# Optimization experiments

Hardware: AMD Instinct MI355X
Metric: run time of the kernel (lower is better)

Reference implementation:

```python
import jax, jax.numpy as jnp
import numpy as np
from jax.scipy.special import logsumexp

ALPHA = 1.0
TOP_K = 128
SK_EPS = 0.001   # sinkhorn entropic epsilon
SK_ITERS = 20    # max_iter (thresh early-exit dropped for jit; 20 fixed iters)
CLIP_MIN = 0.0001


def _cdist(x, y):
    # batched Euclidean distance, safe-sqrt so grad at 0 is 0 (matches torch.cdist subgradient)
    d2 = (jnp.sum(x * x, -1)[..., :, None] + jnp.sum(y * y, -1)[..., None, :]
          - 2.0 * jnp.einsum('bnd,bmd->bnm', x, y))
    d2 = jnp.maximum(d2, 0.0)
    safe = jnp.where(d2 > 0, d2, 1.0)
    return jnp.where(d2 > 0, jnp.sqrt(safe), 0.0)


def _sinkhorn(cost, p, q):
    # log-domain entropic OT with marginals p [B,N], q [B,M]
    logp, logq = jnp.log(p), jnp.log(q)

    def M(u, v):
        return (-cost + u[..., :, None] + v[..., None, :]) / SK_EPS

    def body(carry, _):
        u, v = carry
        u = SK_EPS * (logp - logsumexp(M(u, v), axis=-1)) + u
        v = SK_EPS * (logq - logsumexp(M(u, v), axis=-2)) + v
        return (u, v), None

    u0 = jnp.zeros_like(p)
    v0 = jnp.zeros_like(q)
    (u, v), _ = jax.lax.scan(body, (u0, v0), None, length=SK_ITERS)
    return jnp.exp(M(u, v))  # transport plan gamma [B,N,M]


def setup_inputs() -> dict:
    key = jax.random.key(0)
    ks = jax.random.split(key, 6)
    B, N, M, D = 8, 2048, 2048, 256
    return {
        'src': jax.random.normal(ks[0], (B, N, 3), dtype=jnp.float32),
        'tgt': jax.random.normal(ks[1], (B, M, 3), dtype=jnp.float32),
        'src_feats': jax.random.normal(ks[2], (B, N, D), dtype=jnp.float32),
        'tgt_feats': jax.random.uniform(ks[3], (B, M, D), dtype=jnp.float32),
        'src_o': jax.random.uniform(ks[4], (B, N), dtype=jnp.float32),
        'tgt_o': jax.random.uniform(ks[5], (B, M), dtype=jnp.float32),
    }


def reference(src, tgt, src_feats, tgt_feats, src_o, tgt_o):
    src_pi = src_o / jnp.maximum(jnp.sum(src_o, -1, keepdims=True), CLIP_MIN)
    tgt_pi = tgt_o / jnp.maximum(jnp.sum(tgt_o, -1, keepdims=True), CLIP_MIN)
    cost = _cdist(src_feats, tgt_feats)                       # [B,N,M]
    gamma = _sinkhorn(cost, src_pi, tgt_pi)                   # [B,N,M]
    src_corr = (jnp.einsum('bnm,bmd->bnd', gamma, tgt)
                / jnp.maximum(jnp.sum(gamma, -1, keepdims=True), CLIP_MIN))
    prob = jnp.max(gamma, axis=-1)                            # [B,N]
    _, idx = jax.lax.top_k(prob, TOP_K)                       # [B,K]
    src_k = jnp.take_along_axis(src, idx[:, :, None], axis=1)       # [B,K,3]
    tgt_k = jnp.take_along_axis(src_corr, idx[:, :, None], axis=1)  # [B,K,3]
    alpha2 = ALPHA * ALPHA
    src_edge = _cdist(src_k, src_k)
    tgt_edge = _cdist(tgt_k, tgt_k)
    z = jnp.abs(src_edge - tgt_edge)
    loss = jnp.sum(1.0 - jnp.exp(-0.5 * z * z / alpha2), axis=-1)
    return jnp.mean(loss)
```

## Files before the change

kernel.cpp:

```cpp
#include <hip/hip_runtime.h>
#include <math.h>

#define Bb 8
#define Nn 2048
#define Mm 2048
#define Dd 256
#define TOPK 128
#define SK_ITERS 20
#define NCH 32
#define CHROWS (Nn/NCH)
#define NEG_INIT (-1e30f)
#define SCALE_L2 (-1442.6950408889634f)

__global__ void wl_init_kernel(const float* __restrict__ src_o, const float* __restrict__ tgt_o,
                               float* __restrict__ logp2, float* __restrict__ logq2,
                               float* __restrict__ Ve) {
    __shared__ float lds[8];
    int b = blockIdx.x, t = threadIdx.x;
    int l = t & 63, w = t >> 6;
    float s = 0.f, q = 0.f;
    for (int i = t; i < Nn; i += 256) s += src_o[b * Nn + i];
    for (int i = t; i < Mm; i += 256) q += tgt_o[b * Mm + i];
    for (int o = 32; o; o >>= 1) { s += __shfl_xor(s, o); q += __shfl_xor(q, o); }
    if (l == 0) { lds[w] = s; lds[4 + w] = q; }
    __syncthreads();
    float ssum = fmaxf(lds[0] + lds[1] + lds[2] + lds[3], 1e-4f);
    float qsum = fmaxf(lds[4] + lds[5] + lds[6] + lds[7], 1e-4f);
    float rs = 1.f / ssum, rq = 1.f / qsum;
    for (int i = t; i < Nn; i += 256) logp2[b * Nn + i] = log2f(src_o[b * Nn + i] * rs);
    for (int i = t; i < Mm; i += 256) { logq2[b * Mm + i] = log2f(tgt_o[b * Mm + i] * rq); Ve[b * Mm + i] = 0.f; }
}

__global__ void wl_norms_kernel(const float* __restrict__ feats, float* __restrict__ out) {
    int w = threadIdx.x >> 6, l = threadIdx.x & 63;
    int row = blockIdx.x * 4 + w;
    float4 f = ((const float4*)(feats + (size_t)row * Dd))[l];
    float s = f.x * f.x + f.y * f.y + f.z * f.z + f.w * f.w;
    for (int o = 32; o; o >>= 1) s += __shfl_xor(s, o);
    if (l == 0) out[row] = s;
}

#define BT 128
#define KT 32
#define LDT 132
__global__ __launch_bounds__(256)
void wl_cost_kernel(const float* __restrict__ A, const float* __restrict__ Bf,
                    const float* __restrict__ nx, const float* __restrict__ ny,
                    float* __restrict__ Sc) {
    __shared__ float As[KT][LDT];
    __shared__ float Bs[KT][LDT];
    int b = blockIdx.z;
    int n0 = blockIdx.y * BT, m0 = blockIdx.x * BT;
    const float* Ab = A + (size_t)b * Nn * Dd;
    const float* Bbp = Bf + (size_t)b * Mm * Dd;
    int t = threadIdx.x;
    int w = t >> 6, l = t & 63;
    int tx = (w & 1) * 8 + (l & 7);
    int ty = (w >> 1) * 8 + (l >> 3);
    float acc[8][8] = {};
    for (int k0 = 0; k0 < Dd; k0 += KT) {
        __syncthreads();
#pragma unroll
        for (int i = 0; i < 4; i++) {
            int c = t + 256 * i;
            int row = c >> 3, kc = (c & 7) << 2;
            float4 v = *(const float4*)(Ab + (size_t)(n0 + row) * Dd + k0 + kc);
            As[kc + 0][row] = v.x; As[kc + 1][row] = v.y; As[kc + 2][row] = v.z; As[kc + 3][row] = v.w;
            float4 u = *(const float4*)(Bbp + (size_t)(m0 + row) * Dd + k0 + kc);
            Bs[kc + 0][row] = u.x; Bs[kc + 1][row] = u.y; Bs[kc + 2][row] = u.z; Bs[kc + 3][row] = u.w;
        }
        __syncthreads();
#pragma unroll 4
        for (int k = 0; k < KT; k++) {
            float4 a0 = *(const float4*)&As[k][ty * 8];
            float4 a1 = *(const float4*)&As[k][ty * 8 + 4];
            float4 b0 = *(const float4*)&Bs[k][tx * 8];
            float4 b1 = *(const float4*)&Bs[k][tx * 8 + 4];
            float a[8] = { a0.x, a0.y, a0.z, a0.w, a1.x, a1.y, a1.z, a1.w };
            float bv[8] = { b0.x, b0.y, b0.z, b0.w, b1.x, b1.y, b1.z, b1.w };
#pragma unroll
            for (int i = 0; i < 8; i++)
#pragma unroll
                for (int j = 0; j < 8; j++)
                    acc[i][j] = fmaf(a[i], bv[j], acc[i][j]);
        }
    }
    float nyv[8];
#pragma unroll
    for (int j = 0; j < 8; j++) nyv[j] = ny[b * Mm + m0 + tx * 8 + j];
#pragma unroll
    for (int i = 0; i < 8; i++) {
        int n = n0 + ty * 8 + i;
        float nxv = nx[b * Nn + n];
        float o[8];
#pragma unroll
        for (int j = 0; j < 8; j++) {
            float d2 = nxv + nyv[j] - 2.f * acc[i][j];
            d2 = fmaxf(d2, 0.f);
            float c = d2 > 0.f ? sqrtf(d2) : 0.f;
            o[j] = SCALE_L2 * c;
        }
        float* orow = Sc + ((size_t)b * Nn + n) * Mm + m0 + tx * 8;
        *(float4*)orow = make_float4(o[0], o[1], o[2], o[3]);
        *(float4*)(orow + 4) = make_float4(o[4], o[5], o[6], o[7]);
    }
}

__global__ __launch_bounds__(256)
void wl_u_kernel(const float* __restrict__ Sc, const float* __restrict__ Ve,
                 const float* __restrict__ logp2, float* __restrict__ Ue) {
    int w = threadIdx.x >> 6, l = threadIdx.x & 63;
    int row = blockIdx.x * 4 + w;
    int b = row >> 11;
    const float4* s4 = (const float4*)(Sc + (size_t)row * Mm);
    const float4* v4 = (const float4*)(Ve + (size_t)b * Mm);
    float mx0 = NEG_INIT, mx1 = NEG_INIT, mx2 = NEG_INIT, mx3 = NEG_INIT;
    float sm0 = 0.f, sm1 = 0.f, sm2 = 0.f, sm3 = 0.f;
#pragma unroll
    for (int i = 0; i < 8; i++) {
        int c = l + 64 * i;
        float4 sv = s4[c]; float4 vv = v4[c];
        float t0 = sv.x + vv.x, t1 = sv.y + vv.y, t2 = sv.z + vv.z, t3 = sv.w + vv.w;
        float n0 = fmaxf(mx0, t0); sm0 = sm0 * exp2f(mx0 - n0) + exp2f(t0 - n0); mx0 = n0;
        float n1 = fmaxf(mx1, t1); sm1 = sm1 * exp2f(mx1 - n1) + exp2f(t1 - n1); mx1 = n1;
        float n2 = fmaxf(mx2, t2); sm2 = sm2 * exp2f(mx2 - n2) + exp2f(t2 - n2); mx2 = n2;
        float n3 = fmaxf(mx3, t3); sm3 = sm3 * exp2f(mx3 - n3) + exp2f(t3 - n3); mx3 = n3;
    }
    float mx = fmaxf(fmaxf(mx0, mx1), fmaxf(mx2, mx3));
    float sm = sm0 * exp2f(mx0 - mx) + sm1 * exp2f(mx1 - mx) + sm2 * exp2f(mx2 - mx) + sm3 * exp2f(mx3 - mx);
    for (int o = 32; o; o >>= 1) {
        float om = __shfl_xor(mx, o), os = __shfl_xor(sm, o);
        float nm = fmaxf(mx, om);
        sm = sm * exp2f(mx - nm) + os * exp2f(om - nm);
        mx = nm;
    }
    if (l == 0) Ue[row] = logp2[row] - (mx + log2f(sm));
}

__global__ __launch_bounds__(256)
void wl_v_partial_kernel(const float* __restrict__ Sc, const float* __restrict__ Ue,
                         float* __restrict__ pmx, float* __restrict__ psm) {
    int b = blockIdx.z, ch = blockIdx.y;
    int m0 = blockIdx.x * 1024 + threadIdx.x * 4;
    const float* base = Sc + (size_t)b * Nn * Mm;
    const float* ue = Ue + b * Nn;
    float mx0 = NEG_INIT, mx1 = NEG_INIT, mx2 = NEG_INIT, mx3 = NEG_INIT;
    float sm0 = 0.f, sm1 = 0.f, sm2 = 0.f, sm3 = 0.f;
    int nst = ch * CHROWS;
#pragma unroll 4
    for (int n = nst; n < nst + CHROWS; n++) {
        float u = ue[n];
        float4 sv = *(const float4*)(base + (size_t)n * Mm + m0);
        float t0 = sv.x + u, t1 = sv.y + u, t2 = sv.z + u, t3 = sv.w + u;
        float n0 = fmaxf(mx0, t0); sm0 = sm0 * exp2f(mx0 - n0) + exp2f(t0 - n0); mx0 = n0;
        float n1 = fmaxf(mx1, t1); sm1 = sm1 * exp2f(mx1 - n1) + exp2f(t1 - n1); mx1 = n1;
        float n2 = fmaxf(mx2, t2); sm2 = sm2 * exp2f(mx2 - n2) + exp2f(t2 - n2); mx2 = n2;
        float n3 = fmaxf(mx3, t3); sm3 = sm3 * exp2f(mx3 - n3) + exp2f(t3 - n3); mx3 = n3;
    }
    size_t pi = ((size_t)(b * NCH + ch)) * Mm + m0;
    *(float4*)(pmx + pi) = make_float4(mx0, mx1, mx2, mx3);
    *(float4*)(psm + pi) = make_float4(sm0, sm1, sm2, sm3);
}

__global__ void wl_v_combine_kernel(const float* __restrict__ pmx, const float* __restrict__ psm,
                                    const float* __restrict__ logq2, float* __restrict__ Ve) {
    int idx = blockIdx.x * 256 + threadIdx.x;
    int b = idx >> 11, m = idx & (Mm - 1);
    float mx = NEG_INIT, sm = 0.f;
#pragma unroll
    for (int ch = 0; ch < NCH; ch++) {
        float om = pmx[((size_t)(b * NCH + ch)) * Mm + m];
        float os = psm[((size_t)(b * NCH + ch)) * Mm + m];
        float nm = fmaxf(mx, om);
        sm = sm * exp2f(mx - nm) + os * exp2f(om - nm);
        mx = nm;
    }
    Ve[idx] = logq2[idx] - (mx + log2f(sm));
}

__global__ __launch_bounds__(256)
void wl_finalize_kernel(const float* __restrict__ Sc, const float* __restrict__ Ue,
                        const float* __restrict__ Ve, const float* __restrict__ tgt,
                        float* __restrict__ prob, float* __restrict__ corr) {
    int w = threadIdx.x >> 6, l = threadIdx.x & 63;
    int row = blockIdx.x * 4 + w;
    int b = row >> 11;
    const float4* s4 = (const float4*)(Sc + (size_t)row * Mm);
    const float4* v4 = (const float4*)(Ve + (size_t)b * Mm);
    const float4* tg4 = (const float4*)(tgt + (size_t)b * Mm * 3);
    float mx = NEG_INIT, sm = 0.f, w0 = 0.f, w1 = 0.f, w2 = 0.f;
#pragma unroll
    for (int i = 0; i < 8; i++) {
        int c = l + 64 * i;
        float4 sv = s4[c]; float4 vv = v4[c];
        float4 g0 = tg4[3 * c + 0], g1 = tg4[3 * c + 1], g2 = tg4[3 * c + 2];
        float tt[4] = { sv.x + vv.x, sv.y + vv.y, sv.z + vv.z, sv.w + vv.w };
        float gx[4] = { g0.x, g0.w, g1.z, g2.y };
        float gy[4] = { g0.y, g1.x, g1.w, g2.z };
        float gz[4] = { g0.z, g1.y, g2.x, g2.w };
#pragma unroll
        for (int j = 0; j < 4; j++) {
            float nm = fmaxf(mx, tt[j]);
            float ce = exp2f(mx - nm), e = exp2f(tt[j] - nm);
            sm = sm * ce + e;
            w0 = w0 * ce + e * gx[j];
            w1 = w1 * ce + e * gy[j];
            w2 = w2 * ce + e * gz[j];
            mx = nm;
        }
    }
    for (int o = 32; o; o >>= 1) {
        float om = __shfl_xor(mx, o), os = __shfl_xor(sm, o);
        float o0 = __shfl_xor(w0, o), o1 = __shfl_xor(w1, o), o2 = __shfl_xor(w2, o);
        float nm = fmaxf(mx, om);
        float c1 = exp2f(mx - nm), c2 = exp2f(om - nm);
        sm = sm * c1 + os * c2;
        w0 = w0 * c1 + o0 * c2;
        w1 = w1 * c1 + o1 * c2;
        w2 = w2 * c1 + o2 * c2;
        mx = nm;
    }
    if (l == 0) {
        float scale = exp2f(Ue[row] + mx);
        float rowsum = scale * sm;
        float den = fmaxf(rowsum, 1e-4f);
        prob[row] = scale;
        corr[(size_t)row * 3 + 0] = scale * w0 / den;
        corr[(size_t)row * 3 + 1] = scale * w1 / den;
        corr[(size_t)row * 3 + 2] = scale * w2 / den;
    }
}

__global__ __launch_bounds__(256)
void wl_topk_kernel(const float* __restrict__ prob, int* __restrict__ topk) {
    __shared__ float key[2048];
    __shared__ int val[2048];
    int b = blockIdx.x, t = threadIdx.x;
    for (int i = t; i < 2048; i += 256) { key[i] = prob[b * 2048 + i]; val[i] = i; }
    __syncthreads();
    for (int size = 2; size <= 2048; size <<= 1) {
        for (int stride = size >> 1; stride > 0; stride >>= 1) {
            for (int q = t; q < 1024; q += 256) {
                int i = 2 * q - (q & (stride - 1));
                int j = i + stride;
                bool up = ((i & size) == 0);
                float ki = key[i], kj = key[j];
                int vi = val[i], vj = val[j];
                bool jBetter = (kj > ki) || (kj == ki && vj < vi);
                if (up ? jBetter : !jBetter) {
                    key[i] = kj; key[j] = ki;
                    val[i] = vj; val[j] = vi;
                }
            }
            __syncthreads();
        }
    }
    if (t < TOPK) topk[b * TOPK + t] = val[t];
}

__global__ __launch_bounds__(256)
void wl_edge_kernel(const float* __restrict__ src, const float* __restrict__ corr,
                    const int* __restrict__ topk, float* __restrict__ bloss) {
    __shared__ float sx[TOPK][3];
    __shared__ float tx[TOPK][3];
    __shared__ float lds[4];
    int b = blockIdx.x, t = threadIdx.x;
    if (t < TOPK) {
        int id = topk[b * TOPK + t];
        sx[t][0] = src[((size_t)b * 2048 + id) * 3 + 0];
        sx[t][1] = src[((size_t)b * 2048 + id) * 3 + 1];
        sx[t][2] = src[((size_t)b * 2048 + id) * 3 + 2];
        tx[t][0] = corr[((size_t)b * 2048 + id) * 3 + 0];
        tx[t][1] = corr[((size_t)b * 2048 + id) * 3 + 1];
        tx[t][2] = corr[((size_t)b * 2048 + id) * 3 + 2];
    }
    __syncthreads();
    float acc = 0.f;
    for (int p = t; p < TOPK * TOPK; p += 256) {
        int i = p >> 7, j = p & 127;
        float dx = sx[i][0] - sx[j][0], dy = sx[i][1] - sx[j][1], dz = sx[i][2] - sx[j][2];
        float d2s = dx * dx + dy * dy + dz * dz;
        float ds = d2s > 0.f ? sqrtf(d2s) : 0.f;
        float ex = tx[i][0] - tx[j][0], ey = tx[i][1] - tx[j][1], ez = tx[i][2] - tx[j][2];
        float d2t = ex * ex + ey * ey + ez * ez;
        float dt = d2t > 0.f ? sqrtf(d2t) : 0.f;
        float z = fabsf(ds - dt);
        acc += 1.f - expf(-0.5f * z * z);
    }
    int l = t & 63, w = t >> 6;
    for (int o = 32; o; o >>= 1) acc += __shfl_xor(acc, o);
    if (l == 0) lds[w] = acc;
    __syncthreads();
    if (t == 0) bloss[b] = lds[0] + lds[1] + lds[2] + lds[3];
}

__global__ void wl_final_kernel(const float* __restrict__ bloss, float* __restrict__ out) {
    if (threadIdx.x == 0) {
        float s = 0.f;
        for (int i = 0; i < Bb; i++) s += bloss[i];
        out[0] = s / 1024.f;
    }
}

extern "C" void kernel_launch(void* const* d_in, const int* in_sizes, int n_in,
                              void* d_out, int out_size, void* d_ws, size_t ws_size,
                              hipStream_t stream) {
    (void)in_sizes; (void)n_in; (void)out_size;
    const float* src       = (const float*)d_in[0];
    const float* tgt       = (const float*)d_in[1];
    const float* src_feats = (const float*)d_in[2];
    const float* tgt_feats = (const float*)d_in[3];
    const float* src_o     = (const float*)d_in[4];
    const float* tgt_o     = (const float*)d_in[5];
    float* out = (float*)d_out;

    float* ws = (float*)d_ws;
    size_t off = 0;
    float* Sc    = ws + off; off += (size_t)Bb * Nn * Mm;
    float* Ue    = ws + off; off += Bb * Nn;
    float* Ve    = ws + off; off += Bb * Mm;
    float* logp2 = ws + off; off += Bb * Nn;
    float* logq2 = ws + off; off += Bb * Mm;
    float* nx    = ws + off; off += Bb * Nn;
    float* ny    = ws + off; off += Bb * Mm;
    float* prob  = ws + off; off += Bb * Nn;
    float* corr  = ws + off; off += (size_t)Bb * Nn * 3;
    float* pmx   = ws + off; off += (size_t)Bb * NCH * Mm;
    float* psm   = ws + off; off += (size_t)Bb * NCH * Mm;
    int*   topk  = (int*)(ws + off); off += Bb * TOPK;
    float* bloss = ws + off; off += Bb;
    if (ws_size < off * sizeof(float)) return;

    wl_init_kernel<<<Bb, 256, 0, stream>>>(src_o, tgt_o, logp2, logq2, Ve);
    wl_norms_kernel<<<(Bb * Nn) / 4, 256, 0, stream>>>(src_feats, nx);
    wl_norms_kernel<<<(Bb * Mm) / 4, 256, 0, stream>>>(tgt_feats, ny);
    wl_cost_kernel<<<dim3(Mm / BT, Nn / BT, Bb), 256, 0, stream>>>(src_feats, tgt_feats, nx, ny, Sc);

    for (int it = 0; it < SK_ITERS; it++) {
        wl_u_kernel<<<(Bb * Nn) / 4, 256, 0, stream>>>(Sc, Ve, logp2, Ue);
        wl_v_partial_kernel<<<dim3(Mm / 1024, NCH, Bb), 256, 0, stream>>>(Sc, Ue, pmx, psm);
        wl_v_combine_kernel<<<(Bb * Mm) / 256, 256, 0, stream>>>(pmx, psm, logq2, Ve);
    }

    wl_finalize_kernel<<<(Bb * Nn) / 4, 256, 0, stream>>>(Sc, Ue, Ve, tgt, prob, corr);
    wl_topk_kernel<<<Bb, 256, 0, stream>>>(prob, topk);
    wl_edge_kernel<<<Bb, 256, 0, stream>>>(src, corr, topk, bloss);
    wl_final_kernel<<<1, 64, 0, stream>>>(bloss, out);
}
```

Measured before the change: 1.459 ms.

## Fuse Sinkhorn u-update and v-partial reduction into one pass over cost matrix

Merges the row logsumexp (u update) and the column partial logsumexp into a single kernel, so each iteration reads the 128MB cost matrix once instead of twice. Each wave takes a strip of rows, computes the row LSE, and folds the u-shifted values into per-column running max/sum registers. The partials are merged across waves in LDS, and the chunk count goes to 64 when the workspace is large enough. The v-combine now adds the old V, since the partials are taken relative to it. This uses many registers (64 accumulators plus 32 temporaries per thread) and launches only 256 or 512 blocks, which may reduce occupancy.

Measured after the change: 1.867 ms. 28.0% more time.

```diff
diff --git a/kernel.cpp b/kernel.cpp
--- a/kernel.cpp
+++ b/kernel.cpp
@@ -7,10 +7,16 @@
 #define Dd 256
 #define TOPK 128
 #define SK_ITERS 20
-#define NCH 32
-#define CHROWS (Nn/NCH)
 #define NEG_INIT (-1e30f)
 #define SCALE_L2 (-1442.6950408889634f)
+
+__device__ __forceinline__ void lse_merge(float& m, float& s, float m2, float s2) {
+    float d = m2 - m;
+    float e = exp2f(-fabsf(d));
+    bool up = (d > 0.f);
+    s = up ? fmaf(s, e, s2) : fmaf(s2, e, s);
+    m = up ? m2 : m;
+}
 
 __global__ void wl_init_kernel(const float* __restrict__ src_o, const float* __restrict__ tgt_o,
                                float* __restrict__ logp2, float* __restrict__ logq2,
@@ -106,76 +112,85 @@
     }
 }
 
-__global__ __launch_bounds__(256)
-void wl_u_kernel(const float* __restrict__ Sc, const float* __restrict__ Ve,
-                 const float* __restrict__ logp2, float* __restrict__ Ue) {
-    int w = threadIdx.x >> 6, l = threadIdx.x & 63;
-    int row = blockIdx.x * 4 + w;
-    int b = row >> 11;
-    const float4* s4 = (const float4*)(Sc + (size_t)row * Mm);
-    const float4* v4 = (const float4*)(Ve + (size_t)b * Mm);
-    float mx0 = NEG_INIT, mx1 = NEG_INIT, mx2 = NEG_INIT, mx3 = NEG_INIT;
-    float sm0 = 0.f, sm1 = 0.f, sm2 = 0.f, sm3 = 0.f;
-#pragma unroll
-    for (int i = 0; i < 8; i++) {
-        int c = l + 64 * i;
-        float4 sv = s4[c]; float4 vv = v4[c];
-        float t0 = sv.x + vv.x, t1 = sv.y + vv.y, t2 = sv.z + vv.z, t3 = sv.w + vv.w;
-        float n0 = fmaxf(mx0, t0); sm0 = sm0 * exp2f(mx0 - n0) + exp2f(t0 - n0); mx0 = n0;
-        float n1 = fmaxf(mx1, t1); sm1 = sm1 * exp2f(mx1 - n1) + exp2f(t1 - n1); mx1 = n1;
-        float n2 = fmaxf(mx2, t2); sm2 = sm2 * exp2f(mx2 - n2) + exp2f(t2 - n2); mx2 = n2;
-        float n3 = fmaxf(mx3, t3); sm3 = sm3 * exp2f(mx3 - n3) + exp2f(t3 - n3); mx3 = n3;
-    }
-    float mx = fmaxf(fmaxf(mx0, mx1), fmaxf(mx2, mx3));
-    float sm = sm0 * exp2f(mx0 - mx) + sm1 * exp2f(mx1 - mx) + sm2 * exp2f(mx2 - mx) + sm3 * exp2f(mx3 - mx);
-    for (int o = 32; o; o >>= 1) {
-        float om = __shfl_xor(mx, o), os = __shfl_xor(sm, o);
-        float nm = fmaxf(mx, om);
-        sm = sm * exp2f(mx - nm) + os * exp2f(om - nm);
-        mx = nm;
-    }
-    if (l == 0) Ue[row] = logp2[row] - (mx + log2f(sm));
-}
-
-__global__ __launch_bounds__(256)
-void wl_v_partial_kernel(const float* __restrict__ Sc, const float* __restrict__ Ue,
-                         float* __restrict__ pmx, float* __restrict__ psm) {
-    int b = blockIdx.z, ch = blockIdx.y;
-    int m0 = blockIdx.x * 1024 + threadIdx.x * 4;
-    const float* base = Sc + (size_t)b * Nn * Mm;
-    const float* ue = Ue + b * Nn;
-    float mx0 = NEG_INIT, mx1 = NEG_INIT, mx2 = NEG_INIT, mx3 = NEG_INIT;
-    float sm0 = 0.f, sm1 = 0.f, sm2 = 0.f, sm3 = 0.f;
-    int nst = ch * CHROWS;
-#pragma unroll 4
-    for (int n = nst; n < nst + CHROWS; n++) {
-        float u = ue[n];
-        float4 sv = *(const float4*)(base + (size_t)n * Mm + m0);
-        float t0 = sv.x + u, t1 = sv.y + u, t2 = sv.z + u, t3 = sv.w + u;
-        float n0 = fmaxf(mx0, t0); sm0 = sm0 * exp2f(mx0 - n0) + exp2f(t0 - n0); mx0 = n0;
-        float n1 = fmaxf(mx1, t1); sm1 = sm1 * exp2f(mx1 - n1) + exp2f(t1 - n1); mx1 = n1;
-        float n2 = fmaxf(mx2, t2); sm2 = sm2 * exp2f(mx2 - n2) + exp2f(t2 - n2); mx2 = n2;
-        float n3 = fmaxf(mx3, t3); sm3 = sm3 * exp2f(mx3 - n3) + exp2f(t3 - n3); mx3 = n3;
-    }
-    size_t pi = ((size_t)(b * NCH + ch)) * Mm + m0;
-    *(float4*)(pmx + pi) = make_float4(mx0, mx1, mx2, mx3);
-    *(float4*)(psm + pi) = make_float4(sm0, sm1, sm2, sm3);
+__global__ __launch_bounds__(512, 4)
+void wl_fused_kernel(const float* __restrict__ Sc, const float* __restrict__ Ve,
+                     const float* __restrict__ logp2, float* __restrict__ Ue,
+                     float* __restrict__ pmx, float* __restrict__ psm, int nch) {
+    __shared__ float vlds[2048];
+    __shared__ float pm4[8][512];
+    __shared__ float ps4[8][512];
+    int b = blockIdx.y, ch = blockIdx.x;
+    int t = threadIdx.x, w = t >> 6, l = t & 63;
+
+    ((float4*)vlds)[t] = ((const float4*)(Ve + b * Mm))[t];
+    __syncthreads();
+
+    int chrows = Nn / nch;
+    int rpw = chrows >> 3;
+    int row0 = ch * chrows + w * rpw;
+
+    float cmx[32], csm[32];
+#pragma unroll
+    for (int j = 0; j < 32; j++) { cmx[j] = NEG_INIT; csm[j] = 0.f; }
+
+    for (int r = 0; r < rpw; r++) {
+        int row = row0 + r;
+        const float4* rp = (const float4*)(Sc + ((size_t)b * Nn + row) * Mm);
+        float tv[32];
+#pragma unroll
+        for (int j = 0; j < 8; j++) {
+            float4 sv = rp[l + 64 * j];
+            float4 vv = ((const float4*)vlds)[l + 64 * j];
+            tv[4 * j + 0] = sv.x + vv.x;
+            tv[4 * j + 1] = sv.y + vv.y;
+            tv[4 * j + 2] = sv.z + vv.z;
+            tv[4 * j + 3] = sv.w + vv.w;
+        }
+        float rm = tv[0];
+#pragma unroll
+        for (int j = 1; j < 32; j++) rm = fmaxf(rm, tv[j]);
+        for (int o = 32; o; o >>= 1) rm = fmaxf(rm, __shfl_xor(rm, o));
+        float rs = 0.f;
+#pragma unroll
+        for (int j = 0; j < 32; j++) rs += exp2f(tv[j] - rm);
+        for (int o = 32; o; o >>= 1) rs += __shfl_xor(rs, o);
+        float lp = logp2[b * Nn + row];
+        float lrs = log2f(rs);
+        if (l == 0) Ue[b * Nn + row] = lp - rm - lrs;
+        float C = lp - lrs - rm;
+#pragma unroll
+        for (int j = 0; j < 32; j++) lse_merge(cmx[j], csm[j], tv[j] + C, 1.f);
+    }
+
+    for (int q = 0; q < 4; q++) {
+        __syncthreads();
+#pragma unroll
+        for (int jj = 0; jj < 2; jj++) {
+            int j = 2 * q + jj;
+            *(float4*)&pm4[w][256 * jj + 4 * l] =
+                make_float4(cmx[4 * j + 0], cmx[4 * j + 1], cmx[4 * j + 2], cmx[4 * j + 3]);
+            *(float4*)&ps4[w][256 * jj + 4 * l] =
+                make_float4(csm[4 * j + 0], csm[4 * j + 1], csm[4 * j + 2], csm[4 * j + 3]);
+        }
+        __syncthreads();
+        float m = pm4[0][t], s = ps4[0][t];
+#pragma unroll
+        for (int ww = 1; ww < 8; ww++) lse_merge(m, s, pm4[ww][t], ps4[ww][t]);
+        size_t gi = ((size_t)(b * nch + ch)) * Mm + 512 * q + t;
+        pmx[gi] = m; psm[gi] = s;
+    }
 }
 
 __global__ void wl_v_combine_kernel(const float* __restrict__ pmx, const float* __restrict__ psm,
-                                    const float* __restrict__ logq2, float* __restrict__ Ve) {
+                                    const float* __restrict__ logq2, float* __restrict__ Ve, int nch) {
     int idx = blockIdx.x * 256 + threadIdx.x;
     int b = idx >> 11, m = idx & (Mm - 1);
     float mx = NEG_INIT, sm = 0.f;
-#pragma unroll
-    for (int ch = 0; ch < NCH; ch++) {
-        float om = pmx[((size_t)(b * NCH + ch)) * Mm + m];
-        float os = psm[((size_t)(b * NCH + ch)) * Mm + m];
-        float nm = fmaxf(mx, om);
-        sm = sm * exp2f(mx - nm) + os * exp2f(om - nm);
-        mx = nm;
-    }
-    Ve[idx] = logq2[idx] - (mx + log2f(sm));
+    for (int ch = 0; ch < nch; ch++) {
+        size_t gi = ((size_t)(b * nch + ch)) * Mm + m;
+        lse_merge(mx, sm, pmx[gi], psm[gi]);
+    }
+    Ve[idx] = logq2[idx] + Ve[idx] - mx - log2f(sm);
 }
 
 __global__ __launch_bounds__(256)
@@ -314,6 +329,10 @@
     const float* tgt_o     = (const float*)d_in[5];
     float* out = (float*)d_out;
 
+    size_t fixed = (size_t)Bb * Nn * Mm + 7 * (size_t)Bb * Nn + 3 * (size_t)Bb * Nn
+                 + (size_t)Bb * TOPK + Bb + 64;
+    int nch = (ws_size >= (fixed + 2 * (size_t)Bb * 64 * Mm) * sizeof(float)) ? 64 : 32;
+
     float* ws = (float*)d_ws;
     size_t off = 0;
     float* Sc    = ws + off; off += (size_t)Bb * Nn * Mm;
@@ -325,8 +344,8 @@
     float* ny    = ws + off; off += Bb * Mm;
     float* prob  = ws + off; off += Bb * Nn;
     float* corr  = ws + off; off += (size_t)Bb * Nn * 3;
-    float* pmx   = ws + off; off += (size_t)Bb * NCH * Mm;
-    float* psm   = ws + off; off += (size_t)Bb * NCH * Mm;
+    float* pmx   = ws + off; off += (size_t)Bb * nch * Mm;
+    float* psm   = ws + off; off += (size_t)Bb * nch * Mm;
     int*   topk  = (int*)(ws + off); off += Bb * TOPK;
     float* bloss = ws + off; off += Bb;
     if (ws_size < off * sizeof(float)) return;
@@ -337,9 +356,8 @@
     wl_cost_kernel<<<dim3(Mm / BT, Nn / BT, Bb), 256, 0, stream>>>(src_feats, tgt_feats, nx, ny, Sc);
 
     for (int it = 0; it < SK_ITERS; it++) {
-        wl_u_kernel<<<(Bb * Nn) / 4, 256, 0, stream>>>(Sc, Ve, logp2, Ue);
-        wl_v_partial_kernel<<<dim3(Mm / 1024, NCH, Bb), 256, 0, stream>>>(Sc, Ue, pmx, psm);
-        wl_v_combine_kernel<<<(Bb * Mm) / 256, 256, 0, stream>>>(pmx, psm, logq2, Ve);
+        wl_fused_kernel<<<dim3(nch, Bb), 512, 0, stream>>>(Sc, Ve, logp2, Ue, pmx, psm, nch);
+        wl_v_combine_kernel<<<(Bb * Mm) / 256, 256, 0, stream>>>(pmx, psm, logq2, Ve, nch);
     }
 
     wl_finalize_kernel<<<(Bb * Nn) / 4, 256, 0, stream>>>(Sc, Ue, Ve, tgt, prob, corr);
```

## Compute cost matrix with split-fp16 MFMA instead of scalar FP32 FMA

Applied to the files above, without the earlier changes.

The FP32 SIMT GEMM in the cost kernel is replaced by MFMA 16x16x32 f16 instructions. Each float is split into a high fp16 part and a scaled low fp16 residual, and three MFMA products are accumulated to approximate FP32 precision. Tiles become 64x128, and the output is stored as scalar writes in the MFMA layout. This targets the GEMM portion, which is a small share next to the 20 Sinkhorn passes over the 128MB cost matrix. Precision is slightly reduced, and the uncoalesced-ish scalar stores could add cost.

Result: faster. 1.363 ms (-6.5%).

```diff
diff --git a/kernel.cpp b/kernel.cpp
--- a/kernel.cpp
+++ b/kernel.cpp
@@ -11,6 +11,9 @@
 #define CHROWS (Nn/NCH)
 #define NEG_INIT (-1e30f)
 #define SCALE_L2 (-1442.6950408889634f)
+
+typedef _Float16 half8 __attribute__((ext_vector_type(8)));
+typedef float f32x4 __attribute__((ext_vector_type(4)));
 
 __global__ void wl_init_kernel(const float* __restrict__ src_o, const float* __restrict__ tgt_o,
                                float* __restrict__ logp2, float* __restrict__ logq2,
@@ -40,69 +43,92 @@
     if (l == 0) out[row] = s;
 }
 
-#define BT 128
-#define KT 32
-#define LDT 132
+#define CBM 64
+#define CBN 128
+#define CKT 32
+#define HPITCH 40
 __global__ __launch_bounds__(256)
 void wl_cost_kernel(const float* __restrict__ A, const float* __restrict__ Bf,
                     const float* __restrict__ nx, const float* __restrict__ ny,
                     float* __restrict__ Sc) {
-    __shared__ float As[KT][LDT];
-    __shared__ float Bs[KT][LDT];
+    __shared__ _Float16 Ah[CBM][HPITCH], Al[CBM][HPITCH];
+    __shared__ _Float16 Bh[CBN][HPITCH], Bl[CBN][HPITCH];
     int b = blockIdx.z;
-    int n0 = blockIdx.y * BT, m0 = blockIdx.x * BT;
+    int n0 = blockIdx.y * CBM, m0 = blockIdx.x * CBN;
     const float* Ab = A + (size_t)b * Nn * Dd;
     const float* Bbp = Bf + (size_t)b * Mm * Dd;
-    int t = threadIdx.x;
-    int w = t >> 6, l = t & 63;
-    int tx = (w & 1) * 8 + (l & 7);
-    int ty = (w >> 1) * 8 + (l >> 3);
-    float acc[8][8] = {};
-    for (int k0 = 0; k0 < Dd; k0 += KT) {
+    int t = threadIdx.x, w = t >> 6, l = t & 63;
+
+    f32x4 acc1[8], acc2[8];
+#pragma unroll
+    for (int c = 0; c < 8; c++) {
+        acc1[c] = (f32x4){0.f, 0.f, 0.f, 0.f};
+        acc2[c] = (f32x4){0.f, 0.f, 0.f, 0.f};
+    }
+
+    for (int k0 = 0; k0 < Dd; k0 += CKT) {
         __syncthreads();
 #pragma unroll
+        for (int i = 0; i < 2; i++) {
+            int idx = t + 256 * i;
+            int row = idx >> 3, kc = (idx & 7) << 2;
+            float4 v = *(const float4*)(Ab + (size_t)(n0 + row) * Dd + k0 + kc);
+            float h0 = __uint_as_float(__float_as_uint(v.x) & 0xFFFFE000u);
+            float h1 = __uint_as_float(__float_as_uint(v.y) & 0xFFFFE000u);
+            float h2 = __uint_as_float(__float_as_uint(v.z) & 0xFFFFE000u);
+            float h3 = __uint_as_float(__float_as_uint(v.w) & 0xFFFFE000u);
+            Ah[row][kc + 0] = (_Float16)h0; Al[row][kc + 0] = (_Float16)((v.x - h0) * 2048.f);
+            Ah[row][kc + 1] = (_Float16)h1; Al[row][kc + 1] = (_Float16)((v.y - h1) * 2048.f);
+            Ah[row][kc + 2] = (_Float16)h2; Al[row][kc + 2] = (_Float16)((v.z - h2) * 2048.f);
+            Ah[row][kc + 3] = (_Float16)h3; Al[row][kc + 3] = (_Float16)((v.w - h3) * 2048.f);
+        }
+#pragma unroll
         for (int i = 0; i < 4; i++) {
-            int c = t + 256 * i;
-            int row = c >> 3, kc = (c & 7) << 2;
-            float4 v = *(const float4*)(Ab + (size_t)(n0 + row) * Dd + k0 + kc);
-            As[kc + 0][row] = v.x; As[kc + 1][row] = v.y; As[kc + 2][row] = v.z; As[kc + 3][row] = v.w;
-            float4 u = *(const float4*)(Bbp + (size_t)(m0 + row) * Dd + k0 + kc);
-            Bs[kc + 0][row] = u.x; Bs[kc + 1][row] = u.y; Bs[kc + 2][row] = u.z; Bs[kc + 3][row] = u.w;
+            int idx = t + 256 * i;
+            int row = idx >> 3, kc = (idx & 7) << 2;
+            float4 v = *(const float4*)(Bbp + (size_t)(m0 + row) * Dd + k0 + kc);
+            float h0 = __uint_as_float(__float_as_uint(v.x) & 0xFFFFE000u);
+            float h1 = __uint_as_float(__float_as_uint(v.y) & 0xFFFFE000u);
+            float h2 = __uint_as_float(__float_as_uint(v.z) & 0xFFFFE000u);
+            float h3 = __uint_as_float(__float_as_uint(v.w) & 0xFFFFE000u);
+            Bh[row][kc + 0] = (_Float16)h0; Bl[row][kc + 0] = (_Float16)((v.x - h0) * 2048.f);
+            Bh[row][kc + 1] = (_Float16)h1; Bl[row][kc + 1] = (_Float16)((v.y - h1) * 2048.f);
+            Bh[row][kc + 2] = (_Float16)h2; Bl[row][kc + 2] = (_Float16)((v.z - h2) * 2048.f);
+            Bh[row][kc + 3] = (_Float16)h3; Bl[row][kc + 3] = (_Float16)((v.w - h3) * 2048.f);
         }
         __syncthreads();
-#pragma unroll 4
-        for (int k = 0; k < KT; k++) {
-            float4 a0 = *(const float4*)&As[k][ty * 8];
-            float4 a1 = *(const float4*)&As[k][ty * 8 + 4];
-            float4 b0 = *(const float4*)&Bs[k][tx * 8];
-            float4 b1 = *(const float4*)&Bs[k][tx * 8 + 4];
-            float a[8] = { a0.x, a0.y, a0.z, a0.w, a1.x, a1.y, a1.z, a1.w };
-            float bv[8] = { b0.x, b0.y, b0.z, b0.w, b1.x, b1.y, b1.z, b1.w };
-#pragma unroll
-            for (int i = 0; i < 8; i++)
-#pragma unroll
-                for (int j = 0; j < 8; j++)
-                    acc[i][j] = fmaf(a[i], bv[j], acc[i][j]);
-        }
-    }
-    float nyv[8];
-#pragma unroll
-    for (int j = 0; j < 8; j++) nyv[j] = ny[b * Mm + m0 + tx * 8 + j];
-#pragma unroll
-    for (int i = 0; i < 8; i++) {
-        int n = n0 + ty * 8 + i;
-        float nxv = nx[b * Nn + n];
-        float o[8];
-#pragma unroll
-        for (int j = 0; j < 8; j++) {
-            float d2 = nxv + nyv[j] - 2.f * acc[i][j];
+
+        int arow = w * 16 + (l & 15);
+        int kb = (l >> 4) * 8;
+        half8 ah = *(const half8*)&Ah[arow][kb];
+        half8 al = *(const half8*)&Al[arow][kb];
+#pragma unroll
+        for (int c = 0; c < 8; c++) {
+            int brow = c * 16 + (l & 15);
+            half8 bh = *(const half8*)&Bh[brow][kb];
+            half8 bl = *(const half8*)&Bl[brow][kb];
+            acc1[c] = __builtin_amdgcn_mfma_f32_16x16x32_f16(ah, bh, acc1[c], 0, 0, 0);
+            acc2[c] = __builtin_amdgcn_mfma_f32_16x16x32_f16(ah, bl, acc2[c], 0, 0, 0);
+            acc2[c] = __builtin_amdgcn_mfma_f32_16x16x32_f16(al, bh, acc2[c], 0, 0, 0);
+        }
+    }
+
+    int rbase = n0 + w * 16 + (l >> 4) * 4;
+    float nxv[4];
+#pragma unroll
+    for (int r = 0; r < 4; r++) nxv[r] = nx[b * Nn + rbase + r];
+#pragma unroll
+    for (int c = 0; c < 8; c++) {
+        int col = m0 + c * 16 + (l & 15);
+        float nyv = ny[b * Mm + col];
+#pragma unroll
+        for (int r = 0; r < 4; r++) {
+            float G = acc1[c][r] + acc2[c][r] * (1.f / 2048.f);
+            float d2 = nxv[r] + nyv - 2.f * G;
             d2 = fmaxf(d2, 0.f);
-            float c = d2 > 0.f ? sqrtf(d2) : 0.f;
-            o[j] = SCALE_L2 * c;
-        }
-        float* orow = Sc + ((size_t)b * Nn + n) * Mm + m0 + tx * 8;
-        *(float4*)orow = make_float4(o[0], o[1], o[2], o[3]);
-        *(float4*)(orow + 4) = make_float4(o[4], o[5], o[6], o[7]);
+            float cd = d2 > 0.f ? sqrtf(d2) : 0.f;
+            Sc[((size_t)b * Nn + rbase + r) * Mm + col] = SCALE_L2 * cd;
+        }
     }
 }
 
@@ -334,7 +360,7 @@
     wl_init_kernel<<<Bb, 256, 0, stream>>>(src_o, tgt_o, logp2, logq2, Ve);
     wl_norms_kernel<<<(Bb * Nn) / 4, 256, 0, stream>>>(src_feats, nx);
     wl_norms_kernel<<<(Bb * Mm) / 4, 256, 0, stream>>>(tgt_feats, ny);
-    wl_cost_kernel<<<dim3(Mm / BT, Nn / BT, Bb), 256, 0, stream>>>(src_feats, tgt_feats, nx, ny, Sc);
+    wl_cost_kernel<<<dim3(Mm / CBN, Nn / CBM, Bb), 256, 0, stream>>>(src_feats, tgt_feats, nx, ny, Sc);
 
     for (int it = 0; it < SK_ITERS; it++) {
         wl_u_kernel<<<(Bb * Nn) / 4, 256, 0, stream>>>(Sc, Ve, logp2, Ue);
```
